# Optimization experiments

Measured on AMD Instinct MI355X. Metric: run time of the kernel, lower is better.

## Reference

```python
import jax, jax.numpy as jnp
import numpy as np

USER_NUM = 100000
ITEM_NUM = 50000
N = USER_NUM + ITEM_NUM
EMB = 64
N_LAYERS = 3
N_EDGES = 8000000
EPS = 0.1


def setup_inputs() -> dict:
    key = jax.random.key(0)
    ks = jax.random.split(key, 8)
    return {
        "user_emb": jax.random.normal(ks[0], (USER_NUM, EMB), dtype=jnp.float32),
        "item_emb": jax.random.normal(ks[1], (ITEM_NUM, EMB), dtype=jnp.float32),
        "user_prototypes": jax.random.normal(ks[2], (4000, EMB), dtype=jnp.float32),
        "item_prototypes": jax.random.normal(ks[3], (4000, EMB), dtype=jnp.float32),
        "adj_rows": jax.random.randint(ks[4], (N_EDGES,), 0, N, dtype=jnp.int64)
        if jax.config.jax_enable_x64 else jax.random.randint(ks[4], (N_EDGES,), 0, N, dtype=jnp.int32),
        "adj_cols": jax.random.randint(ks[5], (N_EDGES,), 0, N, dtype=jnp.int64)
        if jax.config.jax_enable_x64 else jax.random.randint(ks[5], (N_EDGES,), 0, N, dtype=jnp.int32),
        "adj_vals": jax.random.uniform(ks[6], (N_EDGES,), dtype=jnp.float32),
        "noise": jax.random.uniform(ks[7], (N_LAYERS, N, EMB), dtype=jnp.float32),
    }


def _spmm(rows, cols, vals, x):
    # sparse [N,N] @ dense [N,EMB] via gather + segment-sum
    return jax.ops.segment_sum(vals[:, None] * x[cols], rows, num_segments=N)


def _l2_normalize(x, eps=1e-12):
    # matches torch F.normalize(dim=-1)
    nrm = jnp.sqrt(jnp.sum(x * x, axis=-1, keepdims=True))
    return x / jnp.maximum(nrm, eps)


def reference(user_emb, item_emb, user_prototypes, item_prototypes,
              adj_rows, adj_cols, adj_vals, noise):
    # perturbed=True path (noise injection each layer)
    ego = jnp.concatenate([user_emb, item_emb], axis=0)  # [N, EMB]
    acc = jnp.zeros_like(ego)
    for k in range(N_LAYERS):
        ego = _spmm(adj_rows, adj_cols, adj_vals, ego)
        ego = ego + jnp.sign(ego) * _l2_normalize(noise[k]) * EPS
        acc = acc + ego
    all_embeddings = acc / N_LAYERS  # mean over stacked layers
    user_all = all_embeddings[:USER_NUM]
    item_all = all_embeddings[USER_NUM:]
    return (user_all, item_all, user_prototypes, item_prototypes)
```

## Files before the change

### kernel.cpp

```cpp
#include <hip/hip_runtime.h>

#define USER_NUM 100000
#define ITEM_NUM 50000
#define NN (USER_NUM + ITEM_NUM)
#define EMB 64
#define N_EDGES 8000000
#define EPS_C 0.1f
#define PROTO 4000

#define BSHIFT 6
#define BROWS 64
#define NB ((NN + BROWS - 1) / BROWS)
#define NSUB 8
#define CAPS 608
#define WIN (NSUB * CAPS)
#define CAP 4608

#define SBSHIFT 9
#define SBROWS 512
#define NSB ((NN + SBROWS - 1) / SBROWS)
#define SCAP 28160
#define SF_STRIDE 16
#define CHS 8192
#define NCH ((N_EDGES + CHS - 1) / CHS)

static __device__ __forceinline__ unsigned short f32_to_bf16_rne(float f) {
    unsigned u = __float_as_uint(f);
    u += 0x7FFFu + ((u >> 16) & 1u);
    return (unsigned short)(u >> 16);
}
static __device__ __forceinline__ float bf16_to_f32(unsigned short h) {
    return __uint_as_float(((unsigned)h) << 16);
}
static __device__ __forceinline__ float bf16_lo(unsigned u) {
    return __uint_as_float(u << 16);
}
static __device__ __forceinline__ float bf16_hi(unsigned u) {
    return __uint_as_float(u & 0xFFFF0000u);
}
static __device__ __forceinline__ unsigned pack_bf16(float lo, float hi) {
    return (unsigned)f32_to_bf16_rne(lo) | ((unsigned)f32_to_bf16_rne(hi) << 16);
}

__global__ __launch_bounds__(256) void concat_bf16_kernel(const float* __restrict__ u,
                                                          const float* __restrict__ it,
                                                          unsigned short* __restrict__ out) {
    long i4 = (long)blockIdx.x * 256 + threadIdx.x;
    const long usz4 = (long)USER_NUM * EMB / 4;
    const long tot4 = (long)NN * EMB / 4;
    if (i4 >= tot4) return;
    const float4* src = (i4 < usz4) ? (const float4*)u : (const float4*)it;
    long j = (i4 < usz4) ? i4 : (i4 - usz4);
    float4 v = src[j];
    ushort4 o;
    o.x = f32_to_bf16_rne(v.x); o.y = f32_to_bf16_rne(v.y);
    o.z = f32_to_bf16_rne(v.z); o.w = f32_to_bf16_rne(v.w);
    ((ushort4*)out)[i4] = o;
}

__global__ __launch_bounds__(256) void chunk_sort_scatter(const int* __restrict__ rows,
                                                          const int* __restrict__ cols,
                                                          const float* __restrict__ vals,
                                                          int* __restrict__ sfill,
                                                          uint2* __restrict__ sbuf) {
    __shared__ unsigned skey[CHS];
    __shared__ unsigned sval[CHS];
    __shared__ int hist[NSB];
    __shared__ int pref[NSB + 1];
    __shared__ int gbase[NSB];
    __shared__ int fill[NSB];

    const int tid   = threadIdx.x;
    const int start = blockIdx.x * CHS;
    const int n     = (start + CHS <= N_EDGES) ? CHS : (N_EDGES - start);
    const int n4    = n >> 2;

    for (int b = tid; b < NSB; b += 256) { hist[b] = 0; fill[b] = 0; }
    __syncthreads();

    const int4* rows4 = (const int4*)(rows + start);
    for (int i = tid; i < n4; i += 256) {
        int4 r = rows4[i];
        atomicAdd(&hist[r.x >> SBSHIFT], 1);
        atomicAdd(&hist[r.y >> SBSHIFT], 1);
        atomicAdd(&hist[r.z >> SBSHIFT], 1);
        atomicAdd(&hist[r.w >> SBSHIFT], 1);
    }
    __syncthreads();

    if (tid < 64) {
        int carry = 0;
        #pragma unroll
        for (int g = 0; g < (NSB + 63) / 64; ++g) {
            int idx = g * 64 + tid;
            int h = (idx < NSB) ? hist[idx] : 0;
            int v = h;
            #pragma unroll
            for (int off = 1; off < 64; off <<= 1) {
                int t = __shfl_up(v, off, 64);
                if (tid >= off) v += t;
            }
            if (idx < NSB) pref[idx] = carry + v - h;
            carry += __shfl(v, 63, 64);
        }
        if (tid == 0) pref[NSB] = carry;
    }
    __syncthreads();

    for (int b = tid; b < NSB; b += 256)
        gbase[b] = hist[b] ? atomicAdd(&sfill[b * SF_STRIDE], hist[b]) : 0;

    const int4*   cols4 = (const int4*)(cols + start);
    const float4* vals4 = (const float4*)(vals + start);
    for (int i = tid; i < n4; i += 256) {
        int4   r = rows4[i];
        int4   c = cols4[i];
        float4 v = vals4[i];
        {
            int b = r.x >> SBSHIFT; int p = pref[b] + atomicAdd(&fill[b], 1);
            skey[p] = ((unsigned)r.x & (SBROWS - 1)) | ((unsigned)c.x << SBSHIFT);
            sval[p] = __float_as_uint(v.x);
        }
        {
            int b = r.y >> SBSHIFT; int p = pref[b] + atomicAdd(&fill[b], 1);
            skey[p] = ((unsigned)r.y & (SBROWS - 1)) | ((unsigned)c.y << SBSHIFT);
            sval[p] = __float_as_uint(v.y);
        }
        {
            int b = r.z >> SBSHIFT; int p = pref[b] + atomicAdd(&fill[b], 1);
            skey[p] = ((unsigned)r.z & (SBROWS - 1)) | ((unsigned)c.z << SBSHIFT);
            sval[p] = __float_as_uint(v.z);
        }
        {
            int b = r.w >> SBSHIFT; int p = pref[b] + atomicAdd(&fill[b], 1);
            skey[p] = ((unsigned)r.w & (SBROWS - 1)) | ((unsigned)c.w << SBSHIFT);
            sval[p] = __float_as_uint(v.w);
        }
    }
    __syncthreads();

    for (int j = tid; j < n; j += 256) {
        int lo = 0, hi = NSB;
        while (hi - lo > 1) {
            int mid = (lo + hi) >> 1;
            if (pref[mid] <= j) lo = mid; else hi = mid;
        }
        int gpos = gbase[lo] + (j - pref[lo]);
        if (gpos < SCAP) {
            uint2 pk; pk.x = skey[j]; pk.y = sval[j];
            sbuf[(size_t)lo * SCAP + gpos] = pk;
        }
    }
}

__global__ __launch_bounds__(512) void bin_rowsort(const int* __restrict__ sfill,
                                                   const uint2* __restrict__ sbuf,
                                                   uint2* __restrict__ dst,
                                                   int* __restrict__ row_start,
                                                   int* __restrict__ row_cnt) {
    __shared__ int hist[SBROWS], pref[SBROWS], fill[SBROWS];
    const int s = blockIdx.x, tid = threadIdx.x;
    int total = sfill[s * SF_STRIDE]; if (total > SCAP) total = SCAP;
    const uint2* src = sbuf + (size_t)s * SCAP;

    for (int r = tid; r < SBROWS; r += 512) { hist[r] = 0; fill[r] = 0; }
    __syncthreads();

    const int n2 = total >> 1;
    const uint4* src4 = (const uint4*)src;
    for (int i = tid; i < n2; i += 512) {
        uint4 q = src4[i];
        atomicAdd(&hist[q.x & (SBROWS - 1)], 1);
        atomicAdd(&hist[q.z & (SBROWS - 1)], 1);
    }
    if (tid == 0 && (total & 1)) atomicAdd(&hist[src[total - 1].x & (SBROWS - 1)], 1);
    __syncthreads();

    if (tid < 64) {
        int carry = 0;
        #pragma unroll
        for (int g = 0; g < SBROWS / 64; ++g) {
            int idx = g * 64 + tid;
            int h = hist[idx];
            int v = h;
            #pragma unroll
            for (int off = 1; off < 64; off <<= 1) {
                int t = __shfl_up(v, off, 64);
                if (tid >= off) v += t;
            }
            pref[idx] = carry + v - h;
            carry += __shfl(v, 63, 64);
        }
    }
    __syncthreads();

    uint2* dwin = dst + (size_t)s * SCAP;
    for (int i = tid; i < n2; i += 512) {
        uint4 q = src4[i];
        {
            int r = (int)(q.x & (SBROWS - 1));
            int p = pref[r] + atomicAdd(&fill[r], 1);
            uint2 o; o.x = q.x >> SBSHIFT; o.y = q.y;
            dwin[p] = o;
        }
        {
            int r = (int)(q.z & (SBROWS - 1));
            int p = pref[r] + atomicAdd(&fill[r], 1);
            uint2 o; o.x = q.z >> SBSHIFT; o.y = q.w;
            dwin[p] = o;
        }
    }
    if (tid == 0 && (total & 1)) {
        uint2 pk = src[total - 1];
        int r = (int)(pk.x & (SBROWS - 1));
        int p = pref[r] + atomicAdd(&fill[r], 1);
        uint2 o; o.x = pk.x >> SBSHIFT; o.y = pk.y;
        dwin[p] = o;
    }
    if (tid < SBROWS) {
        int row = s * SBROWS + tid;
        if (row < NN) { row_start[row] = s * SCAP + pref[tid]; row_cnt[row] = hist[tid]; }
    }
}

__global__ __launch_bounds__(256) void spmm_csr_fused(const int* __restrict__ row_start,
                                                      const int* __restrict__ row_cnt,
                                                      const uint2* __restrict__ csr,
                                                      const unsigned short* __restrict__ x,
                                                      const float* __restrict__ noise_k,
                                                      unsigned short* __restrict__ ego_out,
                                                      float* __restrict__ acc,
                                                      int mode) {
    int row  = (blockIdx.x * 256 + threadIdx.x) >> 6;
    int lane = threadIdx.x & 63;
    if (row >= NN) return;
    const int slot = lane >> 3;
    const int m    = lane & 7;
    const unsigned moff = (unsigned)m << 3;

    int s   = row_start[row];
    int end = s + row_cnt[row];

    float a0 = 0.f, a1 = 0.f, a2 = 0.f, a3 = 0.f;
    float a4 = 0.f, a5 = 0.f, a6 = 0.f, a7 = 0.f;
    float b0 = 0.f, b1 = 0.f, b2 = 0.f, b3 = 0.f;
    float b4 = 0.f, b5 = 0.f, b6 = 0.f, b7 = 0.f;
    int e = s;
    for (; e + 16 <= end; e += 16) {
        uint2 pA = csr[e + slot];
        uint2 pB = csr[e + 8 + slot];
        uint4 gA = *(const uint4*)(x + (((unsigned)pA.x) << 6) + moff);
        uint4 gB = *(const uint4*)(x + (((unsigned)pB.x) << 6) + moff);
        float vA = __uint_as_float(pA.y);
        float vB = __uint_as_float(pB.y);
        a0 += vA * bf16_lo(gA.x); a1 += vA * bf16_hi(gA.x);
        a2 += vA * bf16_lo(gA.y); a3 += vA * bf16_hi(gA.y);
        a4 += vA * bf16_lo(gA.z); a5 += vA * bf16_hi(gA.z);
        a6 += vA * bf16_lo(gA.w); a7 += vA * bf16_hi(gA.w);
        b0 += vB * bf16_lo(gB.x); b1 += vB * bf16_hi(gB.x);
        b2 += vB * bf16_lo(gB.y); b3 += vB * bf16_hi(gB.y);
        b4 += vB * bf16_lo(gB.z); b5 += vB * bf16_hi(gB.z);
        b6 += vB * bf16_lo(gB.w); b7 += vB * bf16_hi(gB.w);
    }
    for (; e < end; e += 8) {
        int idx = e + slot;
        uint2 p = make_uint2(0u, 0u);
        if (idx < end) p = csr[idx];
        uint4 g = *(const uint4*)(x + (((unsigned)p.x) << 6) + moff);
        float v = __uint_as_float(p.y);
        a0 += v * bf16_lo(g.x); a1 += v * bf16_hi(g.x);
        a2 += v * bf16_lo(g.y); a3 += v * bf16_hi(g.y);
        a4 += v * bf16_lo(g.z); a5 += v * bf16_hi(g.z);
        a6 += v * bf16_lo(g.w); a7 += v * bf16_hi(g.w);
    }
    a0 += b0; a1 += b1; a2 += b2; a3 += b3;
    a4 += b4; a5 += b5; a6 += b6; a7 += b7;

    #pragma unroll
    for (int off = 8; off < 64; off <<= 1) {
        a0 += __shfl_xor(a0, off, 64);
        a1 += __shfl_xor(a1, off, 64);
        a2 += __shfl_xor(a2, off, 64);
        a3 += __shfl_xor(a3, off, 64);
        a4 += __shfl_xor(a4, off, 64);
        a5 += __shfl_xor(a5, off, 64);
        a6 += __shfl_xor(a6, off, 64);
        a7 += __shfl_xor(a7, off, 64);
    }

    if (slot == 0) {
        size_t base4 = (size_t)row * 16 + ((unsigned)m << 1);
        float4 n0 = ((const float4*)noise_k)[base4];
        float4 n1 = ((const float4*)noise_k)[base4 + 1];
        float ss = n0.x * n0.x + n0.y * n0.y + n0.z * n0.z + n0.w * n0.w
                 + n1.x * n1.x + n1.y * n1.y + n1.z * n1.z + n1.w * n1.w;
        #pragma unroll
        for (int off = 1; off < 8; off <<= 1) ss += __shfl_xor(ss, off, 64);
        float inv = EPS_C / fmaxf(sqrtf(ss), 1e-12f);

        float e0 = fmaf(((a0 > 0.f) ? 1.f : ((a0 < 0.f) ? -1.f : 0.f)) * n0.x, inv, a0);
        float e1 = fmaf(((a1 > 0.f) ? 1.f : ((a1 < 0.f) ? -1.f : 0.f)) * n0.y, inv, a1);
        float e2 = fmaf(((a2 > 0.f) ? 1.f : ((a2 < 0.f) ? -1.f : 0.f)) * n0.z, inv, a2);
        float e3 = fmaf(((a3 > 0.f) ? 1.f : ((a3 < 0.f) ? -1.f : 0.f)) * n0.w, inv, a3);
        float e4 = fmaf(((a4 > 0.f) ? 1.f : ((a4 < 0.f) ? -1.f : 0.f)) * n1.x, inv, a4);
        float e5 = fmaf(((a5 > 0.f) ? 1.f : ((a5 < 0.f) ? -1.f : 0.f)) * n1.y, inv, a5);
        float e6 = fmaf(((a6 > 0.f) ? 1.f : ((a6 < 0.f) ? -1.f : 0.f)) * n1.z, inv, a6);
        float e7 = fmaf(((a7 > 0.f) ? 1.f : ((a7 < 0.f) ? -1.f : 0.f)) * n1.w, inv, a7);

        uint4 o;
        o.x = pack_bf16(e0, e1); o.y = pack_bf16(e2, e3);
        o.z = pack_bf16(e4, e5); o.w = pack_bf16(e6, e7);
        ((uint4*)ego_out)[(size_t)row * 8 + m] = o;

        float4* accp = (float4*)acc + base4;
        if (mode == 0) {
            accp[0] = make_float4(e0, e1, e2, e3);
            accp[1] = make_float4(e4, e5, e6, e7);
        } else if (mode == 1) {
            float4 c0 = accp[0], c1 = accp[1];
            c0.x += e0; c0.y += e1; c0.z += e2; c0.w += e3;
            c1.x += e4; c1.y += e5; c1.z += e6; c1.w += e7;
            accp[0] = c0; accp[1] = c1;
        } else {
            float4 c0 = accp[0], c1 = accp[1];
            c0.x = (c0.x + e0) * (1.0f / 3.0f); c0.y = (c0.y + e1) * (1.0f / 3.0f);
            c0.z = (c0.z + e2) * (1.0f / 3.0f); c0.w = (c0.w + e3) * (1.0f / 3.0f);
            c1.x = (c1.x + e4) * (1.0f / 3.0f); c1.y = (c1.y + e5) * (1.0f / 3.0f);
            c1.z = (c1.z + e6) * (1.0f / 3.0f); c1.w = (c1.w + e7) * (1.0f / 3.0f);
            accp[0] = c0; accp[1] = c1;
        }
    }
}

__global__ __launch_bounds__(256) void bucket_scatter_fixed(const int* __restrict__ rows,
                                                            const int* __restrict__ cols,
                                                            const float* __restrict__ vals,
                                                            int* __restrict__ bfill,
                                                            uint2* __restrict__ bbuf) {
    int e = blockIdx.x * 256 + threadIdx.x;
    if (e >= N_EDGES) return;
    int sub = blockIdx.x & (NSUB - 1);
    int r = rows[e];
    int b = r >> BSHIFT;
    int pos = atomicAdd(&bfill[b * NSUB + sub], 1);
    if (pos < CAPS) {
        uint2 pk;
        pk.x = (unsigned)(r & (BROWS - 1)) | ((unsigned)cols[e] << BSHIFT);
        pk.y = __float_as_uint(vals[e]);
        bbuf[(size_t)b * WIN + sub * CAPS + pos] = pk;
    }
}

__global__ __launch_bounds__(256) void bucket_sort_fixed(const int* __restrict__ bfill,
                                                         uint2* __restrict__ bbuf,
                                                         int* __restrict__ row_start,
                                                         int* __restrict__ row_cnt) {
    __shared__ uint2 buf[CAP];
    __shared__ int scnt[NSUB], soff[NSUB];
    __shared__ int h[BROWS], pref[BROWS], fill[BROWS];
    int b = blockIdx.x;
    int tid = threadIdx.x;
    if (tid < NSUB) {
        int c = bfill[b * NSUB + tid];
        scnt[tid] = (c < CAPS) ? c : CAPS;
    }
    if (tid < BROWS) { h[tid] = 0; fill[tid] = 0; }
    __syncthreads();
    if (tid == 0) {
        int run = 0;
        #pragma unroll
        for (int s = 0; s < NSUB; ++s) { soff[s] = run; run += scnt[s]; }
    }
    __syncthreads();
    int total = soff[NSUB - 1] + scnt[NSUB - 1];
    if (total > CAP) total = CAP;
    for (int s = 0; s < NSUB; ++s) {
        int c = scnt[s], off = soff[s];
        const uint2* src = bbuf + (size_t)b * WIN + s * CAPS;
        for (int i = tid; i < c; i += 256)
            if (off + i < CAP) buf[off + i] = src[i];
    }
    __syncthreads();
    for (int i = tid; i < total; i += 256) atomicAdd(&h[buf[i].x & (BROWS - 1)], 1);
    __syncthreads();
    if (tid == 0) {
        int run = 0;
        #pragma unroll
        for (int r = 0; r < BROWS; ++r) { pref[r] = run; run += h[r]; }
    }
    __syncthreads();
    uint2* dst = bbuf + (size_t)b * WIN;
    for (int i = tid; i < total; i += 256) {
        unsigned m = buf[i].x;
        int rl = (int)(m & (BROWS - 1));
        int pos = pref[rl] + atomicAdd(&fill[rl], 1);
        uint2 pk;
        pk.x = m >> BSHIFT;
        pk.y = buf[i].y;
        dst[pos] = pk;
    }
    if (tid < BROWS) {
        int row = b * BROWS + tid;
        if (row < NN) { row_start[row] = b * WIN + pref[tid]; row_cnt[row] = h[tid]; }
    }
}

__global__ __launch_bounds__(256) void spmm_csr_old(const int* __restrict__ row_start,
                                                    const int* __restrict__ row_cnt,
                                                    const uint2* __restrict__ csr,
                                                    const unsigned short* __restrict__ x,
                                                    const float* __restrict__ noise_k,
                                                    unsigned short* __restrict__ ego_out,
                                                    float* __restrict__ acc,
                                                    int mode) {
    int row = (blockIdx.x * 256 + threadIdx.x) >> 6;
    int lane = threadIdx.x & 63;
    if (row >= NN) return;
    int s = row_start[row];
    int end = s + row_cnt[row];
    float a0 = 0.f, a1 = 0.f, a2 = 0.f, a3 = 0.f;
    int e = s;
    for (; e + 4 <= end; e += 4) {
        uint2 p0 = csr[e], p1 = csr[e + 1], p2 = csr[e + 2], p3 = csr[e + 3];
        a0 += __uint_as_float(p0.y) * bf16_to_f32(x[(size_t)p0.x * EMB + lane]);
        a1 += __uint_as_float(p1.y) * bf16_to_f32(x[(size_t)p1.x * EMB + lane]);
        a2 += __uint_as_float(p2.y) * bf16_to_f32(x[(size_t)p2.x * EMB + lane]);
        a3 += __uint_as_float(p3.y) * bf16_to_f32(x[(size_t)p3.x * EMB + lane]);
    }
    for (; e < end; ++e) {
        uint2 p = csr[e];
        a0 += __uint_as_float(p.y) * bf16_to_f32(x[(size_t)p.x * EMB + lane]);
    }
    float a = (a0 + a1) + (a2 + a3);
    size_t idx = (size_t)row * EMB + lane;
    float nv = noise_k[idx];
    float ss = nv * nv;
    #pragma unroll
    for (int off = 32; off >= 1; off >>= 1) ss += __shfl_xor(ss, off, 64);
    float nrm = fmaxf(sqrtf(ss), 1e-12f);
    float sgn = (a > 0.0f) ? 1.0f : ((a < 0.0f) ? -1.0f : 0.0f);
    float e1 = a + sgn * (nv / nrm) * EPS_C;
    ego_out[idx] = f32_to_bf16_rne(e1);
    if (mode == 0)      acc[idx] = e1;
    else if (mode == 1) acc[idx] += e1;
    else                acc[idx] = (acc[idx] + e1) * (1.0f / 3.0f);
}

__global__ __launch_bounds__(256) void concat_f32_kernel(const float* __restrict__ u,
                                                         const float* __restrict__ it,
                                                         float* __restrict__ out) {
    long i = (long)blockIdx.x * 256 + threadIdx.x;
    const long usz = (long)USER_NUM * EMB;
    const long tot = (long)NN * EMB;
    if (i >= tot) return;
    out[i] = (i < usz) ? u[i] : it[i - usz];
}

__global__ __launch_bounds__(256) void spmm_atomic_kernel(const int* __restrict__ rows,
                                                          const int* __restrict__ cols,
                                                          const float* __restrict__ vals,
                                                          const float* __restrict__ x,
                                                          float* __restrict__ y) {
    long t = (long)blockIdx.x * 256 + threadIdx.x;
    int e = (int)(t >> 6);
    int lane = (int)(t & 63);
    if (e >= N_EDGES) return;
    atomicAdd(&y[(long)rows[e] * EMB + lane], vals[e] * x[(long)cols[e] * EMB + lane]);
}

__global__ __launch_bounds__(256) void noise_acc_kernel(float* __restrict__ ego,
                                                        const float* __restrict__ noise_k,
                                                        float* __restrict__ acc,
                                                        int mode) {
    long t = (long)blockIdx.x * 256 + threadIdx.x;
    int node = (int)(t >> 6);
    int lane = (int)(t & 63);
    if (node >= NN) return;
    long idx = (long)node * EMB + lane;
    float nv = noise_k[idx];
    float s = nv * nv;
    #pragma unroll
    for (int off = 32; off >= 1; off >>= 1) s += __shfl_xor(s, off, 64);
    float nrm = fmaxf(sqrtf(s), 1e-12f);
    float e0 = ego[idx];
    float sgn = (e0 > 0.0f) ? 1.0f : ((e0 < 0.0f) ? -1.0f : 0.0f);
    float e1 = e0 + sgn * (nv / nrm) * EPS_C;
    ego[idx] = e1;
    if (mode == 0)      acc[idx] = e1;
    else if (mode == 1) acc[idx] += e1;
    else                acc[idx] = (acc[idx] + e1) * (1.0f / 3.0f);
}

extern "C" void kernel_launch(void* const* d_in, const int* in_sizes, int n_in,
                              void* d_out, int out_size, void* d_ws, size_t ws_size,
                              hipStream_t stream) {
    const float* user_emb   = (const float*)d_in[0];
    const float* item_emb   = (const float*)d_in[1];
    const float* user_proto = (const float*)d_in[2];
    const float* item_proto = (const float*)d_in[3];
    const int*   rows       = (const int*)d_in[4];
    const int*   cols       = (const int*)d_in[5];
    const float* vals       = (const float*)d_in[6];
    const float* noise      = (const float*)d_in[7];
    float* out = (float*)d_out;

    const size_t EGO_BF = ((size_t)NN * EMB * sizeof(unsigned short) + 255) & ~(size_t)255;
    const size_t NARR   = ((size_t)NN * sizeof(int) + 255) & ~(size_t)255;

    const size_t SBUF_SZ  = (size_t)NSB * SCAP * sizeof(uint2);
    const size_t DST_SZ   = (size_t)NSB * SCAP * sizeof(uint2);
    const size_t SFILL_SZ = ((size_t)NSB * SF_STRIDE * sizeof(int) + 255) & ~(size_t)255;
    const size_t required_new = 2 * EGO_BF + SBUF_SZ + DST_SZ + 2 * NARR + SFILL_SZ;

    const size_t BBUF   = (size_t)NB * WIN * sizeof(uint2);
    const size_t FARR   = ((size_t)NB * NSUB * sizeof(int) + 255) & ~(size_t)255;
    const size_t required_old = 2 * EGO_BF + BBUF + 2 * NARR + FARR;

    float* acc = out;
    const int elemTotal  = NN * EMB;
    const int elemBlocks = (elemTotal + 255) / 256;
    const int vecBlocks  = (elemTotal / 4 + 255) / 256;
    const int edgeBlocks = (N_EDGES + 255) / 256;
    const int rowWaveBlocks = (NN + 3) / 4;

    if (ws_size >= required_new) {
        char* p = (char*)d_ws;
        unsigned short* egoA = (unsigned short*)p;  p += EGO_BF;
        unsigned short* egoB = (unsigned short*)p;  p += EGO_BF;
        uint2* sbuf          = (uint2*)p;           p += SBUF_SZ;
        uint2* dstbuf        = (uint2*)p;           p += DST_SZ;
        int* row_start       = (int*)p;             p += NARR;
        int* row_cnt         = (int*)p;             p += NARR;
        int* sfill           = (int*)p;             p += SFILL_SZ;

        concat_bf16_kernel<<<vecBlocks, 256, 0, stream>>>(user_emb, item_emb, egoA);
        hipMemsetAsync(sfill, 0, (size_t)NSB * SF_STRIDE * sizeof(int), stream);
        chunk_sort_scatter<<<NCH, 256, 0, stream>>>(rows, cols, vals, sfill, sbuf);
        bin_rowsort<<<NSB, 512, 0, stream>>>(sfill, sbuf, dstbuf, row_start, row_cnt);

        unsigned short* cur = egoA;
        unsigned short* nxt = egoB;
        for (int k = 0; k < 3; ++k) {
            int mode = (k == 0) ? 0 : ((k == 2) ? 2 : 1);
            spmm_csr_fused<<<rowWaveBlocks, 256, 0, stream>>>(
                row_start, row_cnt, dstbuf, cur,
                noise + (size_t)k * NN * EMB, nxt, acc, mode);
            unsigned short* t = cur; cur = nxt; nxt = t;
        }
    } else if (ws_size >= required_old) {
        char* p = (char*)d_ws;
        unsigned short* egoA = (unsigned short*)p;  p += EGO_BF;
        unsigned short* egoB = (unsigned short*)p;  p += EGO_BF;
        uint2* bbuf          = (uint2*)p;           p += BBUF;
        int* row_start       = (int*)p;             p += NARR;
        int* row_cnt         = (int*)p;             p += NARR;
        int* bfill           = (int*)p;             p += FARR;

        concat_bf16_kernel<<<vecBlocks, 256, 0, stream>>>(user_emb, item_emb, egoA);
        hipMemsetAsync(bfill, 0, (size_t)NB * NSUB * sizeof(int), stream);
        bucket_scatter_fixed<<<edgeBlocks, 256, 0, stream>>>(rows, cols, vals, bfill, bbuf);
        bucket_sort_fixed<<<NB, 256, 0, stream>>>(bfill, bbuf, row_start, row_cnt);

        unsigned short* cur = egoA;
        unsigned short* nxt = egoB;
        for (int k = 0; k < 3; ++k) {
            int mode = (k == 0) ? 0 : ((k == 2) ? 2 : 1);
            spmm_csr_old<<<rowWaveBlocks, 256, 0, stream>>>(
                row_start, row_cnt, bbuf, cur,
                noise + (size_t)k * NN * EMB, nxt, acc, mode);
            unsigned short* t = cur; cur = nxt; nxt = t;
        }
    } else {
        const size_t EGO_SZ = (size_t)NN * EMB * sizeof(float);
        float* fA = (float*)d_ws;
        float* fB = (float*)((char*)d_ws + EGO_SZ);
        concat_f32_kernel<<<elemBlocks, 256, 0, stream>>>(user_emb, item_emb, fA);
        float* cur = fA; float* nxt = fB;
        for (int k = 0; k < 3; ++k) {
            hipMemsetAsync(nxt, 0, EGO_SZ, stream);
            spmm_atomic_kernel<<<N_EDGES / 4, 256, 0, stream>>>(rows, cols, vals, cur, nxt);
            int mode = (k == 0) ? 0 : ((k == 2) ? 2 : 1);
            noise_acc_kernel<<<elemBlocks, 256, 0, stream>>>(
                nxt, noise + (size_t)k * NN * EMB, acc, mode);
            float* t = cur; cur = nxt; nxt = t;
        }
    }

    hipMemcpyAsync(out + (size_t)NN * EMB, user_proto,
                   (size_t)PROTO * EMB * sizeof(float), hipMemcpyDeviceToDevice, stream);
    hipMemcpyAsync(out + (size_t)NN * EMB + (size_t)PROTO * EMB, item_proto,
                   (size_t)PROTO * EMB * sizeof(float), hipMemcpyDeviceToDevice, stream);
}
```

Measured before the change: 845.5 us.

## Split edge binning into histogram, global scan, and direct scatter passes

Replaces the single chunk-local sort-and-scatter kernel with three kernels: a per-chunk bin histogram, a per-bin scan across chunks that gives each chunk deterministic global offsets, and a scatter that writes edges straight to global bin buffers. This drops the shared-memory staging arrays, the binary search per element and the global atomics on bin fill counters, and it doubles the chunk size. The cost is an extra pass that reads the rows array again, a histogram matrix in the workspace, and scattered uncoalesced global writes in place of the previously contiguous per-bin runs.

```diff
diff --git a/kernel.cpp b/kernel.cpp
--- a/kernel.cpp
+++ b/kernel.cpp
@@ -21,8 +21,8 @@
 #define NSB ((NN + SBROWS - 1) / SBROWS)
 #define SCAP 28160
 #define SF_STRIDE 16
-#define CHS 8192
-#define NCH ((N_EDGES + CHS - 1) / CHS)
+#define CHS2 16384
+#define NCH2 ((N_EDGES + CHS2 - 1) / CHS2)
 
 static __device__ __forceinline__ unsigned short f32_to_bf16_rne(float f) {
     unsigned u = __float_as_uint(f);
@@ -58,26 +58,15 @@
     ((ushort4*)out)[i4] = o;
 }
 
-__global__ __launch_bounds__(256) void chunk_sort_scatter(const int* __restrict__ rows,
-                                                          const int* __restrict__ cols,
-                                                          const float* __restrict__ vals,
-                                                          int* __restrict__ sfill,
-                                                          uint2* __restrict__ sbuf) {
-    __shared__ unsigned skey[CHS];
-    __shared__ unsigned sval[CHS];
+__global__ __launch_bounds__(256) void chunk_hist(const int* __restrict__ rows,
+                                                  int* __restrict__ histc) {
     __shared__ int hist[NSB];
-    __shared__ int pref[NSB + 1];
-    __shared__ int gbase[NSB];
-    __shared__ int fill[NSB];
-
-    const int tid   = threadIdx.x;
-    const int start = blockIdx.x * CHS;
-    const int n     = (start + CHS <= N_EDGES) ? CHS : (N_EDGES - start);
-    const int n4    = n >> 2;
-
-    for (int b = tid; b < NSB; b += 256) { hist[b] = 0; fill[b] = 0; }
-    __syncthreads();
-
+    const int c = blockIdx.x, tid = threadIdx.x;
+    const int start = c * CHS2;
+    const int n = (start + CHS2 <= N_EDGES) ? CHS2 : (N_EDGES - start);
+    const int n4 = n >> 2;
+    for (int b = tid; b < NSB; b += 256) hist[b] = 0;
+    __syncthreads();
     const int4* rows4 = (const int4*)(rows + start);
     for (int i = tid; i < n4; i += 256) {
         int4 r = rows4[i];
@@ -87,68 +76,84 @@
         atomicAdd(&hist[r.w >> SBSHIFT], 1);
     }
     __syncthreads();
-
-    if (tid < 64) {
-        int carry = 0;
+    for (int b = tid; b < NSB; b += 256) histc[(size_t)c * NSB + b] = hist[b];
+}
+
+__global__ __launch_bounds__(256) void bin_scan(int* __restrict__ histc,
+                                                int* __restrict__ sfill) {
+    int wave = (blockIdx.x * 256 + threadIdx.x) >> 6;
+    int lane = threadIdx.x & 63;
+    if (wave >= NSB) return;
+    int running = 0;
+    for (int i0 = 0; i0 < NCH2; i0 += 64) {
+        int idx = i0 + lane;
+        int v = (idx < NCH2) ? histc[(size_t)idx * NSB + wave] : 0;
+        int incl = v;
         #pragma unroll
-        for (int g = 0; g < (NSB + 63) / 64; ++g) {
-            int idx = g * 64 + tid;
-            int h = (idx < NSB) ? hist[idx] : 0;
-            int v = h;
-            #pragma unroll
-            for (int off = 1; off < 64; off <<= 1) {
-                int t = __shfl_up(v, off, 64);
-                if (tid >= off) v += t;
-            }
-            if (idx < NSB) pref[idx] = carry + v - h;
-            carry += __shfl(v, 63, 64);
-        }
-        if (tid == 0) pref[NSB] = carry;
-    }
-    __syncthreads();
-
-    for (int b = tid; b < NSB; b += 256)
-        gbase[b] = hist[b] ? atomicAdd(&sfill[b * SF_STRIDE], hist[b]) : 0;
-
+        for (int off = 1; off < 64; off <<= 1) {
+            int t = __shfl_up(incl, off, 64);
+            if (lane >= off) incl += t;
+        }
+        if (idx < NCH2) histc[(size_t)idx * NSB + wave] = running + incl - v;
+        running += __shfl(incl, 63, 64);
+    }
+    if (lane == 0) sfill[wave * SF_STRIDE] = running;
+}
+
+__global__ __launch_bounds__(256) void chunk_scatter(const int* __restrict__ rows,
+                                                     const int* __restrict__ cols,
+                                                     const float* __restrict__ vals,
+                                                     const int* __restrict__ offc,
+                                                     uint2* __restrict__ sbuf) {
+    __shared__ int offL[NSB];
+    __shared__ int fill[NSB];
+    const int c = blockIdx.x, tid = threadIdx.x;
+    const int start = c * CHS2;
+    const int n = (start + CHS2 <= N_EDGES) ? CHS2 : (N_EDGES - start);
+    const int n4 = n >> 2;
+    for (int b = tid; b < NSB; b += 256) {
+        offL[b] = offc[(size_t)c * NSB + b];
+        fill[b] = 0;
+    }
+    __syncthreads();
+    const int4*   rows4 = (const int4*)(rows + start);
     const int4*   cols4 = (const int4*)(cols + start);
     const float4* vals4 = (const float4*)(vals + start);
     for (int i = tid; i < n4; i += 256) {
         int4   r = rows4[i];
-        int4   c = cols4[i];
+        int4   cc = cols4[i];
         float4 v = vals4[i];
         {
-            int b = r.x >> SBSHIFT; int p = pref[b] + atomicAdd(&fill[b], 1);
-            skey[p] = ((unsigned)r.x & (SBROWS - 1)) | ((unsigned)c.x << SBSHIFT);
-            sval[p] = __float_as_uint(v.x);
+            int b = r.x >> SBSHIFT; int g = offL[b] + atomicAdd(&fill[b], 1);
+            if (g < SCAP) {
+                uint2 pk; pk.x = ((unsigned)r.x & (SBROWS - 1)) | ((unsigned)cc.x << SBSHIFT);
+                pk.y = __float_as_uint(v.x);
+                sbuf[(size_t)b * SCAP + g] = pk;
+            }
         }
         {
-            int b = r.y >> SBSHIFT; int p = pref[b] + atomicAdd(&fill[b], 1);
-            skey[p] = ((unsigned)r.y & (SBROWS - 1)) | ((unsigned)c.y << SBSHIFT);
-            sval[p] = __float_as_uint(v.y);
+            int b = r.y >> SBSHIFT; int g = offL[b] + atomicAdd(&fill[b], 1);
+            if (g < SCAP) {
+                uint2 pk; pk.x = ((unsigned)r.y & (SBROWS - 1)) | ((unsigned)cc.y << SBSHIFT);
+                pk.y = __float_as_uint(v.y);
+                sbuf[(size_t)b * SCAP + g] = pk;
+            }
         }
         {
-            int b = r.z >> SBSHIFT; int p = pref[b] + atomicAdd(&fill[b], 1);
-            skey[p] = ((unsigned)r.z & (SBROWS - 1)) | ((unsigned)c.z << SBSHIFT);
-            sval[p] = __float_as_uint(v.z);
+            int b = r.z >> SBSHIFT; int g = offL[b] + atomicAdd(&fill[b], 1);
+            if (g < SCAP) {
+                uint2 pk; pk.x = ((unsigned)r.z & (SBROWS - 1)) | ((unsigned)cc.z << SBSHIFT);
+                pk.y = __float_as_uint(v.z);
+                sbuf[(size_t)b * SCAP + g] = pk;
+            }
         }
         {
-            int b = r.w >> SBSHIFT; int p = pref[b] + atomicAdd(&fill[b], 1);
-            skey[p] = ((unsigned)r.w & (SBROWS - 1)) | ((unsigned)c.w << SBSHIFT);
-            sval[p] = __float_as_uint(v.w);
-        }
-    }
-    __syncthreads();
-
-    for (int j = tid; j < n; j += 256) {
-        int lo = 0, hi = NSB;
-        while (hi - lo > 1) {
-            int mid = (lo + hi) >> 1;
-            if (pref[mid] <= j) lo = mid; else hi = mid;
-        }
-        int gpos = gbase[lo] + (j - pref[lo]);
-        if (gpos < SCAP) {
-            uint2 pk; pk.x = skey[j]; pk.y = sval[j];
-            sbuf[(size_t)lo * SCAP + gpos] = pk;
+            int b = r.w >> SBSHIFT; int g = offL[b] + atomicAdd(&fill[b], 1);
+            if (g < SCAP) {
+                uint2 pk; pk.x = ((unsigned)r.w & (SBROWS - 1)) | ((unsigned)cc.w << SBSHIFT);
+                pk.y = __float_as_uint(v.w);
+                sbuf[(size_t)b * SCAP + g] = pk;
+            }
         }
     }
 }
@@ -510,7 +515,8 @@
     const size_t SBUF_SZ  = (size_t)NSB * SCAP * sizeof(uint2);
     const size_t DST_SZ   = (size_t)NSB * SCAP * sizeof(uint2);
     const size_t SFILL_SZ = ((size_t)NSB * SF_STRIDE * sizeof(int) + 255) & ~(size_t)255;
-    const size_t required_new = 2 * EGO_BF + SBUF_SZ + DST_SZ + 2 * NARR + SFILL_SZ;
+    const size_t HISTC_SZ = ((size_t)NCH2 * NSB * sizeof(int) + 255) & ~(size_t)255;
+    const size_t required_new = 2 * EGO_BF + SBUF_SZ + DST_SZ + 2 * NARR + SFILL_SZ + HISTC_SZ;
 
     const size_t BBUF   = (size_t)NB * WIN * sizeof(uint2);
     const size_t FARR   = ((size_t)NB * NSUB * sizeof(int) + 255) & ~(size_t)255;
@@ -522,6 +528,7 @@
     const int vecBlocks  = (elemTotal / 4 + 255) / 256;
     const int edgeBlocks = (N_EDGES + 255) / 256;
     const int rowWaveBlocks = (NN + 3) / 4;
+    const int scanBlocks = (NSB + 3) / 4;
 
     if (ws_size >= required_new) {
         char* p = (char*)d_ws;
@@ -532,10 +539,12 @@
         int* row_start       = (int*)p;             p += NARR;
         int* row_cnt         = (int*)p;             p += NARR;
         int* sfill           = (int*)p;             p += SFILL_SZ;
+        int* histc           = (int*)p;             p += HISTC_SZ;
 
         concat_bf16_kernel<<<vecBlocks, 256, 0, stream>>>(user_emb, item_emb, egoA);
-        hipMemsetAsync(sfill, 0, (size_t)NSB * SF_STRIDE * sizeof(int), stream);
-        chunk_sort_scatter<<<NCH, 256, 0, stream>>>(rows, cols, vals, sfill, sbuf);
+        chunk_hist<<<NCH2, 256, 0, stream>>>(rows, histc);
+        bin_scan<<<scanBlocks, 256, 0, stream>>>(histc, sfill);
+        chunk_scatter<<<NCH2, 256, 0, stream>>>(rows, cols, vals, histc, sbuf);
         bin_rowsort<<<NSB, 512, 0, stream>>>(sfill, sbuf, dstbuf, row_start, row_cnt);
 
         unsigned short* cur = egoA;
```

After: 862.6 us. 1.02x slower.
